# Optimization experiments

Measured on AMD Instinct MI355X. Metric: run time of the kernel, lower is better.

Reference implementation:

```python
import jax, jax.numpy as jnp
import numpy as np

TAU = 0.1  # temperature (registered buffer, non-trainable)
EPS = 1e-12  # F.normalize eps


def setup_inputs() -> dict:
    key = jax.random.key(0)
    k1, k2 = jax.random.split(key)
    B, C = 4096, 512
    z1 = jax.random.normal(k1, (B, C), dtype=jnp.float32)
    z2 = jax.random.normal(k2, (B, C), dtype=jnp.float32)
    return {"z1": z1, "z2": z2}


def _l2_normalize(x):
    # matches F.normalize(p=2, dim=1): x / max(||x||, eps)
    n = jnp.sqrt(jnp.sum(x * x, axis=1, keepdims=True))
    return x / jnp.maximum(n, EPS)


def reference(z1, z2):
    B = z1.shape[0]
    N = 2 * B
    z = jnp.concatenate([_l2_normalize(z1), _l2_normalize(z2)], axis=0)  # [2B, C]
    # cosine similarity of unit vectors == dot product -> single GEMM
    S = jnp.exp((z @ z.T) / TAU)  # [2B, 2B]
    rows = jnp.arange(N)
    pos_cols = (rows + B) % N  # mask[r, c]=1 iff r == (c+B) mod 2B  <=> c == (r+B) mod 2B
    positive = S[rows, pos_cols]                 # [2B]
    # negatives = row sum over ~mask; note the original INCLUDES the diagonal
    negative = jnp.sum(S, axis=1) - positive     # [2B]
    pairs_loss = -jnp.log(positive / negative)   # [2B]
    loss = pairs_loss.reshape(2, B).sum(axis=0) / N  # [B]
    return loss.mean()  # reduce=True
```

## Files before the change

kernel.cpp:

```cpp
#include <hip/hip_runtime.h>
#include <hip/hip_bf16.h>


#define BDIM 4096
#define CDIM 512
#define NROWS 8192

typedef __attribute__((ext_vector_type(4))) float f32x4;
typedef __attribute__((ext_vector_type(8))) short bf16x8;

__device__ __forceinline__ unsigned short f2bf_rne(float x) {
    unsigned u = __float_as_uint(x);
    u += 0x7fffu + ((u >> 16) & 1u);
    return (unsigned short)(u >> 16);
}

__global__ __launch_bounds__(256) void normalize_kernel(
    const float* __restrict__ z1, const float* __restrict__ z2,
    unsigned short* __restrict__ zb, float* __restrict__ pos10) {
    const int w = threadIdx.x >> 6, lane = threadIdx.x & 63;
    const int r = blockIdx.x * 4 + w;
    const float4* p1 = (const float4*)(z1 + (size_t)r * CDIM);
    const float4* p2 = (const float4*)(z2 + (size_t)r * CDIM);
    float4 a0 = p1[lane], a1 = p1[64 + lane];
    float4 b0 = p2[lane], b1 = p2[64 + lane];
    float s1 = a0.x * a0.x + a0.y * a0.y + a0.z * a0.z + a0.w * a0.w +
               a1.x * a1.x + a1.y * a1.y + a1.z * a1.z + a1.w * a1.w;
    float s2 = b0.x * b0.x + b0.y * b0.y + b0.z * b0.z + b0.w * b0.w +
               b1.x * b1.x + b1.y * b1.y + b1.z * b1.z + b1.w * b1.w;
    float d = a0.x * b0.x + a0.y * b0.y + a0.z * b0.z + a0.w * b0.w +
              a1.x * b1.x + a1.y * b1.y + a1.z * b1.z + a1.w * b1.w;
#pragma unroll
    for (int m = 1; m < 64; m <<= 1) {
        s1 += __shfl_xor(s1, m, 64);
        s2 += __shfl_xor(s2, m, 64);
        d += __shfl_xor(d, m, 64);
    }
    const float n1 = fmaxf(sqrtf(s1), 1e-12f);
    const float n2 = fmaxf(sqrtf(s2), 1e-12f);
    const float i1 = 1.0f / n1, i2 = 1.0f / n2;
    ushort4 o;
    ushort4* q1 = (ushort4*)(zb + (size_t)r * CDIM);
    ushort4* q2 = (ushort4*)(zb + (size_t)(r + BDIM) * CDIM);
    o.x = f2bf_rne(a0.x * i1); o.y = f2bf_rne(a0.y * i1);
    o.z = f2bf_rne(a0.z * i1); o.w = f2bf_rne(a0.w * i1);
    q1[lane] = o;
    o.x = f2bf_rne(a1.x * i1); o.y = f2bf_rne(a1.y * i1);
    o.z = f2bf_rne(a1.z * i1); o.w = f2bf_rne(a1.w * i1);
    q1[64 + lane] = o;
    o.x = f2bf_rne(b0.x * i2); o.y = f2bf_rne(b0.y * i2);
    o.z = f2bf_rne(b0.z * i2); o.w = f2bf_rne(b0.w * i2);
    q2[lane] = o;
    o.x = f2bf_rne(b1.x * i2); o.y = f2bf_rne(b1.y * i2);
    o.z = f2bf_rne(b1.z * i2); o.w = f2bf_rne(b1.w * i2);
    q2[64 + lane] = o;
    if (lane == 0) pos10[r] = (d / (n1 * n2)) * 10.0f;
}

__global__ __launch_bounds__(256) void simgemm_kernel(
    const unsigned short* __restrict__ Z, float* __restrict__ rowsum) {
    const int bx = blockIdx.x, by = blockIdx.y;
    if (bx < by) return;
    const bool diag = (bx == by);

    __shared__ unsigned short lds[4][128 * 64];

    const int t = threadIdx.x;
    const int lane = t & 63, w = t >> 6;
    const int wr = w >> 1, wc = w & 1;

    f32x4 acc[4][4] = {};

    const int srow = t >> 3;
    const int scolb = (((t & 7) ^ ((t >> 3) & 7)) << 4);
    const char* Zb = (const char*)Z;
    const size_t apan = ((size_t)(by * 128) << 10);
    const size_t bpan = ((size_t)(bx * 128) << 10);

#define STAGE(k0, db)                                                          \
    {                                                                          \
        const int kb_ = ((k0) << 1) + scolb;                                   \
        _Pragma("unroll") for (int i_ = 0; i_ < 4; ++i_) {                     \
            const size_t ro_ = ((size_t)(i_ * 32 + srow) << 10) + kb_;         \
            __builtin_amdgcn_global_load_lds(                                  \
                (const __attribute__((address_space(1))) void*)(Zb + apan + ro_), \
                (__attribute__((address_space(3))) void*)(lds[(db) * 2] + i_ * 2048 + w * 512), \
                16, 0, 0);                                                     \
            __builtin_amdgcn_global_load_lds(                                  \
                (const __attribute__((address_space(1))) void*)(Zb + bpan + ro_), \
                (__attribute__((address_space(3))) void*)(lds[(db) * 2 + 1] + i_ * 2048 + w * 512), \
                16, 0, 0);                                                     \
        }                                                                      \
    }

    STAGE(0, 0);
    __syncthreads();

    const int sw = (lane & 7) << 4;
#pragma unroll
    for (int it = 0; it < 8; ++it) {
        const int cur = it & 1;
        if (it < 7) STAGE((it + 1) * 64, cur ^ 1);

        const unsigned short* Ab = lds[cur * 2];
        const unsigned short* Bb = lds[cur * 2 + 1];
#pragma unroll
        for (int kk = 0; kk < 2; ++kk) {
            const int koff = (((lane >> 4) << 4) + kk * 64) ^ sw;
            bf16x8 af[4], bfr[4];
#pragma unroll
            for (int mi = 0; mi < 4; ++mi) {
                const int row = wr * 64 + mi * 16 + (lane & 15);
                af[mi] = *(const bf16x8*)((const char*)Ab + row * 128 + koff);
            }
#pragma unroll
            for (int ni = 0; ni < 4; ++ni) {
                const int row = wc * 64 + ni * 16 + (lane & 15);
                bfr[ni] = *(const bf16x8*)((const char*)Bb + row * 128 + koff);
            }
#pragma unroll
            for (int mi = 0; mi < 4; ++mi)
#pragma unroll
                for (int ni = 0; ni < 4; ++ni)
                    acc[mi][ni] = __builtin_amdgcn_mfma_f32_16x16x32_bf16(
                        af[mi], bfr[ni], acc[mi][ni], 0, 0, 0);
        }
        __syncthreads();
    }
#undef STAGE

    const float SC = 14.4269504088896340736f;
    const int g = lane >> 4;
    float cs[4] = {0.f, 0.f, 0.f, 0.f};
#pragma unroll
    for (int mi = 0; mi < 4; ++mi) {
        float rs0 = 0.f, rs1 = 0.f, rs2 = 0.f, rs3 = 0.f;
#pragma unroll
        for (int ni = 0; ni < 4; ++ni) {
            f32x4 a = acc[mi][ni];
            const float e0 = exp2f(a[0] * SC);
            const float e1 = exp2f(a[1] * SC);
            const float e2 = exp2f(a[2] * SC);
            const float e3 = exp2f(a[3] * SC);
            rs0 += e0; rs1 += e1; rs2 += e2; rs3 += e3;
            cs[ni] += (e0 + e1) + (e2 + e3);
        }
#pragma unroll
        for (int m = 1; m < 16; m <<= 1) {
            rs0 += __shfl_xor(rs0, m, 64);
            rs1 += __shfl_xor(rs1, m, 64);
            rs2 += __shfl_xor(rs2, m, 64);
            rs3 += __shfl_xor(rs3, m, 64);
        }
        if ((lane & 15) == 0) {
            const int rbase = by * 128 + wr * 64 + mi * 16 + g * 4;
            atomicAdd(&rowsum[rbase + 0], rs0);
            atomicAdd(&rowsum[rbase + 1], rs1);
            atomicAdd(&rowsum[rbase + 2], rs2);
            atomicAdd(&rowsum[rbase + 3], rs3);
        }
    }
    if (!diag) {
#pragma unroll
        for (int ni = 0; ni < 4; ++ni) {
            float c = cs[ni];
            c += __shfl_xor(c, 16, 64);
            c += __shfl_xor(c, 32, 64);
            if (lane < 16)
                atomicAdd(&rowsum[bx * 128 + wc * 64 + ni * 16 + lane], c);
        }
    }
}

__global__ __launch_bounds__(256) void finalize_kernel(
    const float* __restrict__ rowsum, const float* __restrict__ pos10,
    float* __restrict__ out) {
    __shared__ float sm[4];
    const int w = threadIdx.x >> 6, lane = threadIdx.x & 63;
    const int r = blockIdx.x * 256 + threadIdx.x;
    const float p10 = pos10[r];
    const float pos = expf(p10);
    float l = (logf(rowsum[r] - pos) - p10) +
              (logf(rowsum[r + BDIM] - pos) - p10);
#pragma unroll
    for (int m = 1; m < 64; m <<= 1) l += __shfl_xor(l, m, 64);
    if (lane == 0) sm[w] = l;
    __syncthreads();
    if (threadIdx.x == 0) {
        const float tot = sm[0] + sm[1] + sm[2] + sm[3];
        atomicAdd(out, tot * (1.0f / ((float)NROWS * (float)BDIM)));
    }
}

extern "C" void kernel_launch(void* const* d_in, const int* in_sizes, int n_in,
                              void* d_out, int out_size, void* d_ws, size_t ws_size,
                              hipStream_t stream) {
    const float* z1 = (const float*)d_in[0];
    const float* z2 = (const float*)d_in[1];
    float* out = (float*)d_out;
    unsigned short* zb = (unsigned short*)d_ws;
    float* rowsum = (float*)((char*)d_ws + (size_t)NROWS * CDIM * 2);
    float* pos10 = rowsum + NROWS;

    hipMemsetAsync(rowsum, 0, NROWS * sizeof(float), stream);
    hipMemsetAsync(out, 0, sizeof(float), stream);

    normalize_kernel<<<BDIM / 4, 256, 0, stream>>>(z1, z2, zb, pos10);
    dim3 g2(64, 64);
    simgemm_kernel<<<g2, 256, 0, stream>>>(zb, rowsum);
    finalize_kernel<<<BDIM / 256, 256, 0, stream>>>(rowsum, pos10, out);
}
```

Baseline: 154.8 us.

## Use 256x256 GEMM tiles with triangular launch and fold memsets into normalize

The similarity GEMM moves from 128x128 tiles on a 64x64 grid, where blocks below the diagonal exit early, to 256x256 tiles with 512 threads launched only over the 528 upper-triangular tiles. The tile index is decoded from a linear block id. Synchronisation switches to explicit vmcnt waits and s_barrier so the next stage's loads can stay in flight, and the rowsum/out zeroing moves from two memsets into the normalize kernel. Larger tiles raise operand reuse and cut launch overhead, at the cost of more registers and LDS per block and fewer blocks to spread across CUs.

```diff
diff --git a/kernel.cpp b/kernel.cpp
--- a/kernel.cpp
+++ b/kernel.cpp
@@ -5,6 +5,8 @@
 #define BDIM 4096
 #define CDIM 512
 #define NROWS 8192
+#define NTILE 32
+#define NBLK 528
 
 typedef __attribute__((ext_vector_type(4))) float f32x4;
 typedef __attribute__((ext_vector_type(8))) short bf16x8;
@@ -17,7 +19,13 @@
 
 __global__ __launch_bounds__(256) void normalize_kernel(
     const float* __restrict__ z1, const float* __restrict__ z2,
-    unsigned short* __restrict__ zb, float* __restrict__ pos10) {
+    unsigned short* __restrict__ zb, float* __restrict__ pos10,
+    float* __restrict__ rowsum, float* __restrict__ out) {
+    if (blockIdx.x == 0) {
+#pragma unroll
+        for (int i = 0; i < NROWS / 256; ++i) rowsum[i * 256 + threadIdx.x] = 0.f;
+        if (threadIdx.x == 0) out[0] = 0.f;
+    }
     const int w = threadIdx.x >> 6, lane = threadIdx.x & 63;
     const int r = blockIdx.x * 4 + w;
     const float4* p1 = (const float4*)(z1 + (size_t)r * CDIM);
@@ -57,75 +65,81 @@
     if (lane == 0) pos10[r] = (d / (n1 * n2)) * 10.0f;
 }
 
-__global__ __launch_bounds__(256) void simgemm_kernel(
+__global__ __launch_bounds__(512, 2) void simgemm_kernel(
     const unsigned short* __restrict__ Z, float* __restrict__ rowsum) {
-    const int bx = blockIdx.x, by = blockIdx.y;
-    if (bx < by) return;
+    int by = 0, rem = blockIdx.x;
+    while (rem >= NTILE - by) { rem -= NTILE - by; ++by; }
+    const int bx = by + rem;
     const bool diag = (bx == by);
 
-    __shared__ unsigned short lds[4][128 * 64];
+    __shared__ unsigned short lds[2][2][256 * 64];
 
     const int t = threadIdx.x;
     const int lane = t & 63, w = t >> 6;
-    const int wr = w >> 1, wc = w & 1;
-
-    f32x4 acc[4][4] = {};
+    const int wr = w >> 2, wc = w & 3;
+
+    f32x4 acc[8][4] = {};
 
     const int srow = t >> 3;
     const int scolb = (((t & 7) ^ ((t >> 3) & 7)) << 4);
     const char* Zb = (const char*)Z;
-    const size_t apan = ((size_t)(by * 128) << 10);
-    const size_t bpan = ((size_t)(bx * 128) << 10);
-
-#define STAGE(k0, db)                                                          \
-    {                                                                          \
-        const int kb_ = ((k0) << 1) + scolb;                                   \
-        _Pragma("unroll") for (int i_ = 0; i_ < 4; ++i_) {                     \
-            const size_t ro_ = ((size_t)(i_ * 32 + srow) << 10) + kb_;         \
-            __builtin_amdgcn_global_load_lds(                                  \
+    const size_t apan = ((size_t)(by * 256) << 10);
+    const size_t bpan = ((size_t)(bx * 256) << 10);
+
+#define STAGE(kt, db)                                                             \
+    {                                                                             \
+        const int kb_ = ((kt) << 7) + scolb;                                      \
+        _Pragma("unroll") for (int i_ = 0; i_ < 4; ++i_) {                        \
+            const size_t ro_ = ((size_t)(i_ * 64 + srow) << 10) + kb_;            \
+            __builtin_amdgcn_global_load_lds(                                     \
                 (const __attribute__((address_space(1))) void*)(Zb + apan + ro_), \
-                (__attribute__((address_space(3))) void*)(lds[(db) * 2] + i_ * 2048 + w * 512), \
-                16, 0, 0);                                                     \
-            __builtin_amdgcn_global_load_lds(                                  \
+                (__attribute__((address_space(3))) void*)((char*)&lds[db][0][0] + i_ * 8192 + w * 1024), \
+                16, 0, 0);                                                        \
+            __builtin_amdgcn_global_load_lds(                                     \
                 (const __attribute__((address_space(1))) void*)(Zb + bpan + ro_), \
-                (__attribute__((address_space(3))) void*)(lds[(db) * 2 + 1] + i_ * 2048 + w * 512), \
-                16, 0, 0);                                                     \
-        }                                                                      \
+                (__attribute__((address_space(3))) void*)((char*)&lds[db][1][0] + i_ * 8192 + w * 1024), \
+                16, 0, 0);                                                        \
+        }                                                                         \
     }
 
     STAGE(0, 0);
-    __syncthreads();
-
-    const int sw = (lane & 7) << 4;
+    asm volatile("s_waitcnt vmcnt(0)\n\ts_barrier" ::: "memory");
+
+    const int swz = (lane & 7) << 4;
 #pragma unroll
     for (int it = 0; it < 8; ++it) {
         const int cur = it & 1;
-        if (it < 7) STAGE((it + 1) * 64, cur ^ 1);
-
-        const unsigned short* Ab = lds[cur * 2];
-        const unsigned short* Bb = lds[cur * 2 + 1];
+        if (it < 7) {
+            STAGE(it + 1, cur ^ 1);
+            asm volatile("s_waitcnt vmcnt(8)\n\ts_barrier" ::: "memory");
+        } else {
+            asm volatile("s_waitcnt vmcnt(0)\n\ts_barrier" ::: "memory");
+        }
+
+        const char* Ab = (const char*)&lds[cur][0][0];
+        const char* Bb = (const char*)&lds[cur][1][0];
 #pragma unroll
         for (int kk = 0; kk < 2; ++kk) {
-            const int koff = (((lane >> 4) << 4) + kk * 64) ^ sw;
-            bf16x8 af[4], bfr[4];
-#pragma unroll
-            for (int mi = 0; mi < 4; ++mi) {
-                const int row = wr * 64 + mi * 16 + (lane & 15);
-                af[mi] = *(const bf16x8*)((const char*)Ab + row * 128 + koff);
+            const int koff = (kk * 64 + ((lane >> 4) << 4)) ^ swz;
+            bf16x8 af[8], bfr[4];
+#pragma unroll
+            for (int mi = 0; mi < 8; ++mi) {
+                const int row = wr * 128 + mi * 16 + (lane & 15);
+                af[mi] = *(const bf16x8*)(Ab + row * 128 + koff);
             }
 #pragma unroll
             for (int ni = 0; ni < 4; ++ni) {
                 const int row = wc * 64 + ni * 16 + (lane & 15);
-                bfr[ni] = *(const bf16x8*)((const char*)Bb + row * 128 + koff);
+                bfr[ni] = *(const bf16x8*)(Bb + row * 128 + koff);
             }
 #pragma unroll
-            for (int mi = 0; mi < 4; ++mi)
+            for (int mi = 0; mi < 8; ++mi)
 #pragma unroll
                 for (int ni = 0; ni < 4; ++ni)
                     acc[mi][ni] = __builtin_amdgcn_mfma_f32_16x16x32_bf16(
                         af[mi], bfr[ni], acc[mi][ni], 0, 0, 0);
         }
-        __syncthreads();
+        asm volatile("s_barrier" ::: "memory");
     }
 #undef STAGE
 
@@ -133,7 +147,7 @@
     const int g = lane >> 4;
     float cs[4] = {0.f, 0.f, 0.f, 0.f};
 #pragma unroll
-    for (int mi = 0; mi < 4; ++mi) {
+    for (int mi = 0; mi < 8; ++mi) {
         float rs0 = 0.f, rs1 = 0.f, rs2 = 0.f, rs3 = 0.f;
 #pragma unroll
         for (int ni = 0; ni < 4; ++ni) {
@@ -153,7 +167,7 @@
             rs3 += __shfl_xor(rs3, m, 64);
         }
         if ((lane & 15) == 0) {
-            const int rbase = by * 128 + wr * 64 + mi * 16 + g * 4;
+            const int rbase = by * 256 + wr * 128 + mi * 16 + g * 4;
             atomicAdd(&rowsum[rbase + 0], rs0);
             atomicAdd(&rowsum[rbase + 1], rs1);
             atomicAdd(&rowsum[rbase + 2], rs2);
@@ -167,7 +181,7 @@
             c += __shfl_xor(c, 16, 64);
             c += __shfl_xor(c, 32, 64);
             if (lane < 16)
-                atomicAdd(&rowsum[bx * 128 + wc * 64 + ni * 16 + lane], c);
+                atomicAdd(&rowsum[bx * 256 + wc * 64 + ni * 16 + lane], c);
         }
     }
 }
@@ -202,11 +216,7 @@
     float* rowsum = (float*)((char*)d_ws + (size_t)NROWS * CDIM * 2);
     float* pos10 = rowsum + NROWS;
 
-    hipMemsetAsync(rowsum, 0, NROWS * sizeof(float), stream);
-    hipMemsetAsync(out, 0, sizeof(float), stream);
-
-    normalize_kernel<<<BDIM / 4, 256, 0, stream>>>(z1, z2, zb, pos10);
-    dim3 g2(64, 64);
-    simgemm_kernel<<<g2, 256, 0, stream>>>(zb, rowsum);
+    normalize_kernel<<<BDIM / 4, 256, 0, stream>>>(z1, z2, zb, pos10, rowsum, out);
+    simgemm_kernel<<<NBLK, 512, 0, stream>>>(zb, rowsum);
     finalize_kernel<<<BDIM / 256, 256, 0, stream>>>(rowsum, pos10, out);
 }
```

New measurement: 142.0 us. -8.2%, faster.
